# Performance work log

Measured on AMD Instinct MI355X. Metric: run time of the kernel, lower is better.

The kernel has to match this reference:

```python
import jax, jax.numpy as jnp
import numpy as np

N = 50000      # nodes
E = 800000     # edges
CIN = 128
CH = 128
COUT = 64
EPS = 1e-5     # BatchNorm eps


def setup_inputs() -> dict:
    key = jax.random.key(0)
    ks = jax.random.split(key, 16)
    s = 0.1  # weight scale for numerical stability
    return {
        "x": jax.random.normal(ks[0], (N, CIN), jnp.float32),
        "edge_index": jax.random.randint(ks[1], (2, E), 0, N, jnp.int32),
        "edge_weights": jax.random.uniform(ks[2], (E,), jnp.float32),
        "w1": jax.random.normal(ks[3], (CIN, CH), jnp.float32) * s,
        "b1": jnp.zeros((CH,), jnp.float32),
        "bn1_g": jnp.ones((CH,), jnp.float32),
        "bn1_b": jnp.zeros((CH,), jnp.float32),
        "bn1_m": jax.random.normal(ks[4], (CH,), jnp.float32) * 0.1,
        "bn1_v": jax.random.uniform(ks[5], (CH,), jnp.float32) + 0.5,
        "conv_ws": jax.random.normal(ks[6], (2, CH, CH), jnp.float32) * s,
        "conv_bs": jnp.zeros((2, CH), jnp.float32),
        "bns_g": jnp.ones((2, CH), jnp.float32),
        "bns_b": jnp.zeros((2, CH), jnp.float32),
        "bns_m": jax.random.normal(ks[7], (2, CH), jnp.float32) * 0.1,
        "bns_v": jax.random.uniform(ks[8], (2, CH), jnp.float32) + 0.5,
        "lin1_w": jax.random.normal(ks[9], (CH, CH), jnp.float32) * s,
        "lin1_b": jnp.zeros((CH,), jnp.float32),
        "lin2_w": jax.random.normal(ks[10], (CH, COUT), jnp.float32) * s,
        "lin2_b": jnp.zeros((COUT,), jnp.float32),
    }


def _bn(h, g, b, m, v):
    # BatchNorm1d in eval mode: running statistics
    return (h - m) * jax.lax.rsqrt(v + EPS) * g + b


def _gcn(h, w, b, src, dst, norm, n):
    # GCNConv: out[dst] += norm_e * (h @ W)[src]  (self loops already in src/dst)
    h = h @ w
    msg = h[src] * norm[:, None]                 # [E+N, CH]
    return jax.ops.segment_sum(msg, dst, num_segments=n) + b


def reference(x, edge_index, edge_weights, w1, b1, bn1_g, bn1_b, bn1_m, bn1_v,
              conv_ws, conv_bs, bns_g, bns_b, bns_m, bns_v,
              lin1_w, lin1_b, lin2_w, lin2_b):
    n = x.shape[0]
    loop = jnp.arange(n, dtype=edge_index.dtype)
    src = jnp.concatenate([edge_index[0], loop])
    dst = jnp.concatenate([edge_index[1], loop])
    ew = jnp.concatenate([edge_weights, jnp.ones((n,), edge_weights.dtype)])
    # symmetric degree normalization (PyG gcn_norm)
    deg = jax.ops.segment_sum(ew, dst, num_segments=n)
    dis = jnp.where(deg > 0, jax.lax.rsqrt(deg), 0.0)
    norm = dis[src] * ew * dis[dst]

    lrelu = jax.nn.leaky_relu  # slope 0.01, matches F.leaky_relu default
    h = lrelu(_bn(_gcn(x, w1, b1, src, dst, norm, n), bn1_g, bn1_b, bn1_m, bn1_v))
    for i in range(conv_ws.shape[0]):
        h = lrelu(_bn(_gcn(h, conv_ws[i], conv_bs[i], src, dst, norm, n),
                      bns_g[i], bns_b[i], bns_m[i], bns_v[i]) + h)
    h = lrelu(h @ lin1_w + lin1_b)
    # dropout is identity in eval mode
    return h @ lin2_w + lin2_b
```

## Files before the change

### kernel.cpp

```cpp
#include <hip/hip_runtime.h>
#include <hip/hip_bf16.h>


constexpr int   NN    = 50000;
constexpr int   EE    = 800000;
constexpr int   CH    = 128;
constexpr int   SLOTS = 64;
constexpr int   NBUK  = 782;
constexpr int   RCAP  = 2048;
constexpr int   EPB   = 2048;
constexpr int   NB_BIN = (EE + EPB - 1) / EPB;
constexpr int   NB_WZ  = (73728 + 384 + 255) / 256;
constexpr float EPS   = 1e-5f;

typedef __attribute__((ext_vector_type(8))) short bf16x8;
typedef __attribute__((ext_vector_type(4))) float f32x4;
typedef unsigned long long u64;
typedef unsigned short u16;

__device__ inline u16 f2bf_rne(float f) {
  unsigned u = __float_as_uint(f);
  unsigned r = u + 0x7fffu + ((u >> 16) & 1u);
  return (u16)(r >> 16);
}
__device__ inline float bf2f(unsigned h16) {
  return __uint_as_float(h16 << 16);
}


__global__ __launch_bounds__(256) void binw_kernel(
    const int* __restrict__ ei, const float* __restrict__ ew,
    unsigned* __restrict__ gcur, u64* __restrict__ bins,
    const float* __restrict__ w1, const float* __restrict__ bn1_g, const float* __restrict__ bn1_v,
    const float* __restrict__ conv_ws, const float* __restrict__ bns_g, const float* __restrict__ bns_v,
    const float* __restrict__ lin1_w, const float* __restrict__ lin2_w,
    const float* __restrict__ b1, const float* __restrict__ bn1_b, const float* __restrict__ bn1_m,
    const float* __restrict__ conv_bs, const float* __restrict__ bns_b, const float* __restrict__ bns_m,
    u16* __restrict__ w1h, u16* __restrict__ w1l,
    u16* __restrict__ c0h, u16* __restrict__ c0l,
    u16* __restrict__ c1h, u16* __restrict__ c1l,
    u16* __restrict__ l1h, u16* __restrict__ l1l,
    u16* __restrict__ l2h, u16* __restrict__ l2l,
    float* __restrict__ beff)
{
  const int tid = threadIdx.x;
  if (blockIdx.x >= NB_BIN) {
    int idx = (blockIdx.x - NB_BIN) * 256 + tid;
    if (idx >= 73728) {
      int r = idx - 73728;
      if (r >= 384) return;
      int l = r >> 7, c = r & 127;
      float bc, gg, bb, mm, vv;
      if (l == 0) { bc = b1[c]; gg = bn1_g[c]; bb = bn1_b[c]; mm = bn1_m[c]; vv = bn1_v[c]; }
      else {
        int o = (l - 1) * 128 + c;
        bc = conv_bs[o]; gg = bns_g[o]; bb = bns_b[o]; mm = bns_m[o]; vv = bns_v[o];
      }
      beff[r] = (bc - mm) * gg * rsqrtf(vv + EPS) + bb;
      return;
    }
    const float* W; const float* g = nullptr; const float* v = nullptr;
    u16 *hi, *lo; int CO = 128; int local;
    if      (idx < 16384) { W = w1;              g = bn1_g;     v = bn1_v;     hi = w1h; lo = w1l; local = idx; }
    else if (idx < 32768) { W = conv_ws;         g = bns_g;     v = bns_v;     hi = c0h; lo = c0l; local = idx - 16384; }
    else if (idx < 49152) { W = conv_ws + 16384; g = bns_g+128; v = bns_v+128; hi = c1h; lo = c1l; local = idx - 32768; }
    else if (idx < 65536) { W = lin1_w;                                        hi = l1h; lo = l1l; local = idx - 49152; }
    else                  { W = lin2_w;                                        hi = l2h; lo = l2l; local = idx - 65536; CO = 64; }
    int k = local / CO, n = local % CO;
    float w = W[local];
    if (g) w *= g[n] * rsqrtf(v[n] + EPS);
    int NCT = CO / 16;
    int kchunk = k >> 5, kin = k & 31, quad = kin >> 3, j = kin & 7;
    int ct = n >> 4, l = (quad << 4) | (n & 15);
    size_t pos = ((size_t)(kchunk * NCT + ct) * 64 + l) * 8 + j;
    u16 h = f2bf_rne(w);
    hi[pos] = h;
    lo[pos] = f2bf_rne(w - bf2f(h));
    return;
  }
  __shared__ unsigned cnt[NBUK];
  __shared__ unsigned base[NBUK];
  for (int b = tid; b < NBUK; b += 256) cnt[b] = 0;
  __syncthreads();
  const int e0 = blockIdx.x * EPB;
  unsigned pk[8]; u16 bkt[8]; u16 rnk[8]; unsigned char dl[8];
  #pragma unroll
  for (int i = 0; i < 8; i++) {
    int e = e0 + i * 256 + tid;
    if (e < EE) {
      int s = ei[e], d = ei[EE + e];
      float w = ew[e];
      bkt[i] = (u16)(d >> 6);
      dl[i]  = (unsigned char)(d & 63);
      pk[i]  = ((unsigned)f2bf_rne(w) << 16) | (unsigned)s;
      rnk[i] = (u16)atomicAdd(&cnt[bkt[i]], 1u);
    } else bkt[i] = 0xffffu;
  }
  __syncthreads();
  for (int b = tid; b < NBUK; b += 256) {
    unsigned c = cnt[b];
    base[b] = c ? atomicAdd(&gcur[b * 16], c) : 0u;
  }
  __syncthreads();
  #pragma unroll
  for (int i = 0; i < 8; i++) {
    if (bkt[i] == 0xffffu) continue;
    unsigned pos = base[bkt[i]] + rnk[i];
    if (pos < RCAP)
      bins[(size_t)bkt[i] * RCAP + pos] = ((u64)dl[i] << 32) | pk[i];
  }
}


__global__ __launch_bounds__(256) void scatgemm_kernel(
    const unsigned* __restrict__ gcur, const u64* __restrict__ bins,
    unsigned* __restrict__ ell, float* __restrict__ dis,
    const float* __restrict__ Ain,
    const u16* __restrict__ Whi, const u16* __restrict__ Wlo,
    u16* __restrict__ Cout)
{
  __shared__ unsigned rank[64];
  __shared__ float    wsum[64];
  __shared__ float    disl[64];
  __shared__ float    lds[64][CH + 4];
  const int b   = blockIdx.x;
  const int tid = threadIdx.x;

  if (tid < 64) { rank[tid] = 1u; wsum[tid] = 0.f; }
  __syncthreads();
  unsigned cnt = gcur[b * 16];
  if (cnt > RCAP) cnt = RCAP;
  const u64* src = bins + (size_t)b * RCAP;
  for (unsigned i = tid; i < cnt; i += 256) {
    u64 v = src[i];
    unsigned pk = (unsigned)v;
    unsigned dl = (unsigned)(v >> 32);
    unsigned r = atomicAdd(&rank[dl], 1u);
    if (r < SLOTS)
      ell[((size_t)(b * 64 + dl)) * SLOTS + r] = pk;
    atomicAdd(&wsum[dl], bf2f(pk >> 16));
  }
  __syncthreads();
  if (tid < 64) {
    int node = b * 64 + tid;
    float d = rsqrtf(1.0f + wsum[tid]);
    disl[tid] = d;
    if (node < NN) {
      unsigned c = rank[tid];
      if (c > SLOTS) c = SLOTS;
      ell[(size_t)node * SLOTS] = c;
      dis[node] = d;
    }
  }
  __syncthreads();

  const int wave = tid >> 6;
  const int lane = tid & 63;
  const int quad = lane >> 4;
  const int mrow = lane & 15;
  const int row0 = b * 64;

  int arow = row0 + wave * 16 + mrow;
  if (arow >= NN) arow = NN - 1;

  bf16x8 ahi[4], alo[4];
  const float* Ar = Ain + (size_t)arow * CH;
  #pragma unroll
  for (int c = 0; c < 4; c++) {
    int off = c * 32 + quad * 8;
    float4 f0 = *(const float4*)(Ar + off);
    float4 f1 = *(const float4*)(Ar + off + 4);
    float f[8] = {f0.x, f0.y, f0.z, f0.w, f1.x, f1.y, f1.z, f1.w};
    #pragma unroll
    for (int j = 0; j < 8; j++) {
      u16 h = f2bf_rne(f[j]);
      ahi[c][j] = (short)h;
      alo[c][j] = (short)f2bf_rne(f[j] - bf2f(h));
    }
  }

  f32x4 acc[8];
  #pragma unroll
  for (int t = 0; t < 8; t++) acc[t] = (f32x4){0.f, 0.f, 0.f, 0.f};
  #pragma unroll
  for (int c = 0; c < 4; c++) {
    #pragma unroll
    for (int t = 0; t < 8; t++) {
      size_t base = ((size_t)(c * 8 + t) * 64 + lane) * 8;
      bf16x8 bh = *(const bf16x8*)(Whi + base);
      bf16x8 bl = *(const bf16x8*)(Wlo + base);
      acc[t] = __builtin_amdgcn_mfma_f32_16x16x32_bf16(ahi[c], bh, acc[t], 0, 0, 0);
      acc[t] = __builtin_amdgcn_mfma_f32_16x16x32_bf16(alo[c], bh, acc[t], 0, 0, 0);
      acc[t] = __builtin_amdgcn_mfma_f32_16x16x32_bf16(ahi[c], bl, acc[t], 0, 0, 0);
    }
  }

  #pragma unroll
  for (int t = 0; t < 8; t++)
    #pragma unroll
    for (int r = 0; r < 4; r++)
      lds[wave * 16 + quad * 4 + r][t * 16 + mrow] = acc[t][r];
  __syncthreads();

  #pragma unroll
  for (int i = tid; i < 64 * CH / 4; i += 256) {
    int row = (i * 4) / CH;
    int col = (i * 4) % CH;
    int grow = row0 + row;
    if (grow >= NN) continue;
    float rs = disl[row];
    const float* lp = &lds[row][col];
    u16* cp = (u16*)Cout + (size_t)grow * CH + col;
    unsigned p0 = ((unsigned)f2bf_rne(lp[1] * rs) << 16) | f2bf_rne(lp[0] * rs);
    unsigned p1 = ((unsigned)f2bf_rne(lp[3] * rs) << 16) | f2bf_rne(lp[2] * rs);
    *(uint2*)cp = make_uint2(p0, p1);
  }
}

template<bool RES, bool WH>
__device__ __forceinline__ void gather4_qw(
    const u16* __restrict__ hwin, const unsigned* __restrict__ ell,
    const float* __restrict__ dis, const float* __restrict__ beff,
    const u16* __restrict__ res, u16* __restrict__ hout,
    unsigned* __restrict__ hsbase,
    int nbase, int lane, int sub, int grp)
{
  int nd0 = nbase < NN ? nbase : NN - 1;
  unsigned wcur = ell[(size_t)nd0 * SLOTS + lane];
  for (int r = 0; r < 4; r++) {
    int node = nbase + r;
    int nd = node < NN ? node : NN - 1;
    unsigned myword = wcur;
    if (r < 3) {
      int n2 = node + 1 < NN ? node + 1 : NN - 1;
      wcur = ell[(size_t)n2 * SLOTS + lane];
    }
    int cnt = __shfl((int)myword, 0);
    if (cnt > SLOTS) cnt = SLOTS;
    float a[8] = {0.f, 0.f, 0.f, 0.f, 0.f, 0.f, 0.f, 0.f};
    for (int j = 0; j < cnt; j += 32) {
      unsigned sidx[8]; float wv[8];
      #pragma unroll
      for (int q = 0; q < 8; q++) {
        int jj = j + q * 4 + grp;
        unsigned e = (unsigned)__shfl((int)myword, jj & 63);
        float    w = (jj == 0) ? 1.0f : bf2f(e >> 16);
        unsigned s = (jj == 0) ? (unsigned)nd : (e & 0xffffu);
        if (jj >= cnt) { w = 0.f; s = (unsigned)nd; }
        sidx[q] = s; wv[q] = w;
      }
      uint4 h[8];
      #pragma unroll
      for (int q = 0; q < 8; q++)
        h[q] = *(const uint4*)(hwin + (size_t)sidx[q] * CH + sub * 8);
      __builtin_amdgcn_sched_group_barrier(0x20 , 8, 0);
      #pragma unroll
      for (int q = 0; q < 8; q++) {
        float w = wv[q];
        a[0] = fmaf(w, bf2f(h[q].x & 0xffffu), a[0]); a[1] = fmaf(w, bf2f(h[q].x >> 16), a[1]);
        a[2] = fmaf(w, bf2f(h[q].y & 0xffffu), a[2]); a[3] = fmaf(w, bf2f(h[q].y >> 16), a[3]);
        a[4] = fmaf(w, bf2f(h[q].z & 0xffffu), a[4]); a[5] = fmaf(w, bf2f(h[q].z >> 16), a[5]);
        a[6] = fmaf(w, bf2f(h[q].w & 0xffffu), a[6]); a[7] = fmaf(w, bf2f(h[q].w >> 16), a[7]);
      }
    }
    #pragma unroll
    for (int k = 0; k < 8; k++) {
      a[k] += __shfl_xor(a[k], 16);
      a[k] += __shfl_xor(a[k], 32);
    }
    if (grp == 0) {
      float disd = dis[nd];
      int c = sub * 8;
      float4 be0 = *(const float4*)(beff + c);
      float4 be1 = *(const float4*)(beff + c + 4);
      float y[8];
      y[0] = a[0] * disd + be0.x; y[1] = a[1] * disd + be0.y;
      y[2] = a[2] * disd + be0.z; y[3] = a[3] * disd + be0.w;
      y[4] = a[4] * disd + be1.x; y[5] = a[5] * disd + be1.y;
      y[6] = a[6] * disd + be1.z; y[7] = a[7] * disd + be1.w;
      if constexpr (RES) {
        uint4 rr = *(const uint4*)(res + (size_t)nd * CH + c);
        y[0] += bf2f(rr.x & 0xffffu); y[1] += bf2f(rr.x >> 16);
        y[2] += bf2f(rr.y & 0xffffu); y[3] += bf2f(rr.y >> 16);
        y[4] += bf2f(rr.z & 0xffffu); y[5] += bf2f(rr.z >> 16);
        y[6] += bf2f(rr.w & 0xffffu); y[7] += bf2f(rr.w >> 16);
      }
      #pragma unroll
      for (int k = 0; k < 8; k++) y[k] = y[k] > 0.f ? y[k] : 0.01f * y[k];
      uint4 o;
      o.x = ((unsigned)f2bf_rne(y[1]) << 16) | f2bf_rne(y[0]);
      o.y = ((unsigned)f2bf_rne(y[3]) << 16) | f2bf_rne(y[2]);
      o.z = ((unsigned)f2bf_rne(y[5]) << 16) | f2bf_rne(y[4]);
      o.w = ((unsigned)f2bf_rne(y[7]) << 16) | f2bf_rne(y[6]);
      if constexpr (WH) {
        if (node < NN) *(uint4*)(hout + (size_t)node * CH + c) = o;
      }
      *(uint4*)&hsbase[r * 68 + sub * 4] = o;
    }
  }
}

template<bool RES>
__global__ __launch_bounds__(256, 4) void fuse_kernel(
    const u16* __restrict__ hwin,
    const unsigned* __restrict__ ell, const float* __restrict__ dis,
    const float* __restrict__ beff, const u16* __restrict__ res,
    const u16* __restrict__ Whi, const u16* __restrict__ Wlo,
    u16* __restrict__ hout, u16* __restrict__ hwout)
{
  __shared__ unsigned hs[16][68];
  const int tid  = threadIdx.x;
  const int wave = tid >> 6;
  const int lane = tid & 63;
  const int sub  = lane & 15;
  const int grp  = lane >> 4;
  const int row0 = blockIdx.x * 16;

  gather4_qw<RES, true>(hwin, ell, dis, beff, res, hout,
                        &hs[wave * 4][0], row0 + wave * 4, lane, sub, grp);
  __syncthreads();

  bf16x8 af[4];
  #pragma unroll
  for (int c = 0; c < 4; c++)
    af[c] = *(const bf16x8*)&hs[sub][c * 16 + grp * 4];
  __syncthreads();

  f32x4 acc[2];
  #pragma unroll
  for (int t = 0; t < 2; t++) acc[t] = (f32x4){0.f, 0.f, 0.f, 0.f};
  #pragma unroll
  for (int c = 0; c < 4; c++) {
    #pragma unroll
    for (int t = 0; t < 2; t++) {
      size_t base = ((size_t)(c * 8 + wave * 2 + t) * 64 + lane) * 8;
      bf16x8 bh = *(const bf16x8*)(Whi + base);
      bf16x8 bl = *(const bf16x8*)(Wlo + base);
      acc[t] = __builtin_amdgcn_mfma_f32_16x16x32_bf16(af[c], bh, acc[t], 0, 0, 0);
      acc[t] = __builtin_amdgcn_mfma_f32_16x16x32_bf16(af[c], bl, acc[t], 0, 0, 0);
    }
  }

  u16* hs16 = (u16*)&hs[0][0];
  #pragma unroll
  for (int r = 0; r < 4; r++) {
    int row = grp * 4 + r;
    float rs = dis[row0 + row];
    #pragma unroll
    for (int t = 0; t < 2; t++)
      hs16[row * 136 + wave * 32 + t * 16 + sub] = f2bf_rne(acc[t][r] * rs);
  }
  __syncthreads();
  {
    int row   = tid >> 4;
    int chunk = tid & 15;
    uint4 o = *(const uint4*)(hs16 + row * 136 + chunk * 8);
    *(uint4*)(hwout + (size_t)(row0 + row) * CH + chunk * 8) = o;
  }
}

__global__ __launch_bounds__(256, 4) void fuse_last_kernel(
    const u16* __restrict__ hwin,
    const unsigned* __restrict__ ell, const float* __restrict__ dis,
    const float* __restrict__ beff, const u16* __restrict__ res,
    const u16* __restrict__ l1h, const u16* __restrict__ l1l,
    const float* __restrict__ b1,
    const u16* __restrict__ l2h, const u16* __restrict__ l2l,
    const float* __restrict__ b2, float* __restrict__ out)
{
  __shared__ unsigned hs[16][68];
  __shared__ float    fs[16][132];
  const int tid  = threadIdx.x;
  const int wave = tid >> 6;
  const int lane = tid & 63;
  const int sub  = lane & 15;
  const int grp  = lane >> 4;
  const int row0 = blockIdx.x * 16;

  gather4_qw<true, false>(hwin, ell, dis, beff, res, nullptr,
                          &hs[wave * 4][0], row0 + wave * 4, lane, sub, grp);
  __syncthreads();

  bf16x8 af[4];
  #pragma unroll
  for (int c = 0; c < 4; c++)
    af[c] = *(const bf16x8*)&hs[sub][c * 16 + grp * 4];

  f32x4 acc[2];
  #pragma unroll
  for (int t = 0; t < 2; t++) acc[t] = (f32x4){0.f, 0.f, 0.f, 0.f};
  #pragma unroll
  for (int c = 0; c < 4; c++) {
    #pragma unroll
    for (int t = 0; t < 2; t++) {
      size_t base = ((size_t)(c * 8 + wave * 2 + t) * 64 + lane) * 8;
      bf16x8 bh = *(const bf16x8*)(l1h + base);
      bf16x8 bl = *(const bf16x8*)(l1l + base);
      acc[t] = __builtin_amdgcn_mfma_f32_16x16x32_bf16(af[c], bh, acc[t], 0, 0, 0);
      acc[t] = __builtin_amdgcn_mfma_f32_16x16x32_bf16(af[c], bl, acc[t], 0, 0, 0);
    }
  }
  #pragma unroll
  for (int t = 0; t < 2; t++) {
    int col = wave * 32 + t * 16 + sub;
    float bb = b1[col];
    #pragma unroll
    for (int r = 0; r < 4; r++) {
      float x = acc[t][r] + bb;
      x = x > 0.f ? x : 0.01f * x;
      fs[grp * 4 + r][col] = x;
    }
  }
  __syncthreads();

  f32x4 acc2 = (f32x4){0.f, 0.f, 0.f, 0.f};
  #pragma unroll
  for (int c = 0; c < 4; c++) {
    bf16x8 ahi, alo;
    const float* lp = &fs[sub][c * 32 + grp * 8];
    float4 f0 = *(const float4*)lp;
    float4 f1 = *(const float4*)(lp + 4);
    float f[8] = {f0.x, f0.y, f0.z, f0.w, f1.x, f1.y, f1.z, f1.w};
    #pragma unroll
    for (int j = 0; j < 8; j++) {
      u16 h = f2bf_rne(f[j]);
      ahi[j] = (short)h;
      alo[j] = (short)f2bf_rne(f[j] - bf2f(h));
    }
    size_t base = ((size_t)(c * 4 + wave) * 64 + lane) * 8;
    bf16x8 bh = *(const bf16x8*)(l2h + base);
    bf16x8 bl = *(const bf16x8*)(l2l + base);
    acc2 = __builtin_amdgcn_mfma_f32_16x16x32_bf16(ahi, bh, acc2, 0, 0, 0);
    acc2 = __builtin_amdgcn_mfma_f32_16x16x32_bf16(alo, bh, acc2, 0, 0, 0);
    acc2 = __builtin_amdgcn_mfma_f32_16x16x32_bf16(ahi, bl, acc2, 0, 0, 0);
  }
  {
    float bb = b2[wave * 16 + sub];
    #pragma unroll
    for (int r = 0; r < 4; r++) {
      int grow = row0 + grp * 4 + r;
      if (grow < NN)
        out[(size_t)grow * 64 + wave * 16 + sub] = acc2[r] + bb;
    }
  }
}


extern "C" void kernel_launch(void* const* d_in, const int* in_sizes, int n_in,
                              void* d_out, int out_size, void* d_ws, size_t ws_size,
                              hipStream_t stream) {
  const float* x       = (const float*)d_in[0];
  const int*   ei      = (const int*)  d_in[1];
  const float* ew      = (const float*)d_in[2];
  const float* w1      = (const float*)d_in[3];
  const float* b1      = (const float*)d_in[4];
  const float* bn1_g   = (const float*)d_in[5];
  const float* bn1_b   = (const float*)d_in[6];
  const float* bn1_m   = (const float*)d_in[7];
  const float* bn1_v   = (const float*)d_in[8];
  const float* conv_ws = (const float*)d_in[9];
  const float* conv_bs = (const float*)d_in[10];
  const float* bns_g   = (const float*)d_in[11];
  const float* bns_b   = (const float*)d_in[12];
  const float* bns_m   = (const float*)d_in[13];
  const float* bns_v   = (const float*)d_in[14];
  const float* lin1_w  = (const float*)d_in[15];
  const float* lin1_b  = (const float*)d_in[16];
  const float* lin2_w  = (const float*)d_in[17];
  const float* lin2_b  = (const float*)d_in[18];
  float* out = (float*)d_out;

  size_t off = 0;
  auto alloc = [&](size_t elems) -> void* {
    void* p = (char*)d_ws + off * 4;
    off += (elems + 3) & ~(size_t)3;
    return p;
  };
  unsigned* gcur = (unsigned*)alloc(NBUK * 16);
  u64*      bins = (u64*)     alloc((size_t)NBUK * RCAP * 2);
  unsigned* ell  = (unsigned*)alloc((size_t)NN * SLOTS);
  float*    dis  = (float*)   alloc(NN);
  float*    beff = (float*)   alloc(3 * CH);
  u16*      hwa  = (u16*)     alloc((size_t)NN * CH / 2);
  u16*      hwb  = (u16*)     alloc((size_t)NN * CH / 2);
  u16*      h1   = (u16*)     alloc((size_t)NN * CH / 2);
  u16*      h2   = (u16*)     alloc((size_t)NN * CH / 2);
  u16* w1h = (u16*)alloc(CH * CH / 2); u16* w1l = (u16*)alloc(CH * CH / 2);
  u16* c0h = (u16*)alloc(CH * CH / 2); u16* c0l = (u16*)alloc(CH * CH / 2);
  u16* c1h = (u16*)alloc(CH * CH / 2); u16* c1l = (u16*)alloc(CH * CH / 2);
  u16* l1h = (u16*)alloc(CH * CH / 2); u16* l1l = (u16*)alloc(CH * CH / 2);
  u16* l2h = (u16*)alloc(CH * 64 / 2); u16* l2l = (u16*)alloc(CH * 64 / 2);

  const int nb_fuse = (NN + 15) / 16;
  dim3 B(256);

  hipMemsetAsync(gcur, 0, NBUK * 16 * sizeof(unsigned), stream);

  binw_kernel<<<NB_BIN + NB_WZ, B, 0, stream>>>(ei, ew, gcur, bins,
      w1, bn1_g, bn1_v, conv_ws, bns_g, bns_v, lin1_w, lin2_w,
      b1, bn1_b, bn1_m, conv_bs, bns_b, bns_m,
      w1h, w1l, c0h, c0l, c1h, c1l, l1h, l1l, l2h, l2l, beff);

  scatgemm_kernel<<<NBUK, B, 0, stream>>>(gcur, bins, ell, dis, x, w1h, w1l, hwa);

  fuse_kernel<false><<<nb_fuse, B, 0, stream>>>(hwa, ell, dis, beff, nullptr,
      c0h, c0l, h1, hwb);

  fuse_kernel<true><<<nb_fuse, B, 0, stream>>>(hwb, ell, dis, beff + CH, h1,
      c1h, c1l, h2, hwa);

  fuse_last_kernel<<<nb_fuse, B, 0, stream>>>(hwa, ell, dis, beff + 2 * CH, h2,
      l1h, l1l, lin1_b, l2h, l2l, lin2_b, out);
}
```

Baseline: 303.2 us.

## Split gathered feature matrix into two 64-column halves for cache-friendlier gathers

Stores the transformed node features (h@W scaled) as two separate N×64 planes instead of one N×128 array, and gathers each half in a separate pass with 8-byte loads per lane. The intent is to shrink the working set touched by the random neighbour gather in each pass so it fits better in L2/MALL and to reduce register pressure, which also lets launch bounds rise to 6 blocks per SM. The trade-off is that the edge list is walked twice, a block-wide barrier is added inside the gather helper, and the bounds clamp on the last nodes is removed.

Result: slower. 358.7 us (+18.3%).

```diff
diff --git a/kernel.cpp b/kernel.cpp
--- a/kernel.cpp
+++ b/kernel.cpp
@@ -12,6 +12,7 @@
 constexpr int   NB_BIN = (EE + EPB - 1) / EPB;
 constexpr int   NB_WZ  = (73728 + 384 + 255) / 256;
 constexpr float EPS   = 1e-5f;
+constexpr size_t HHALF = (size_t)NN * 64;
 
 typedef __attribute__((ext_vector_type(8))) short bf16x8;
 typedef __attribute__((ext_vector_type(4))) float f32x4;
@@ -210,7 +211,8 @@
     if (grow >= NN) continue;
     float rs = disl[row];
     const float* lp = &lds[row][col];
-    u16* cp = (u16*)Cout + (size_t)grow * CH + col;
+    int half = col >> 6, lcol = col & 63;
+    u16* cp = Cout + (size_t)half * HHALF + (size_t)grow * 64 + lcol;
     unsigned p0 = ((unsigned)f2bf_rne(lp[1] * rs) << 16) | f2bf_rne(lp[0] * rs);
     unsigned p1 = ((unsigned)f2bf_rne(lp[3] * rs) << 16) | f2bf_rne(lp[2] * rs);
     *(uint2*)cp = make_uint2(p0, p1);
@@ -218,90 +220,85 @@
 }
 
 template<bool RES, bool WH>
-__device__ __forceinline__ void gather4_qw(
+__device__ __forceinline__ void gather4_split(
     const u16* __restrict__ hwin, const unsigned* __restrict__ ell,
     const float* __restrict__ dis, const float* __restrict__ beff,
     const u16* __restrict__ res, u16* __restrict__ hout,
     unsigned* __restrict__ hsbase,
     int nbase, int lane, int sub, int grp)
 {
-  int nd0 = nbase < NN ? nbase : NN - 1;
-  unsigned wcur = ell[(size_t)nd0 * SLOTS + lane];
-  for (int r = 0; r < 4; r++) {
-    int node = nbase + r;
-    int nd = node < NN ? node : NN - 1;
-    unsigned myword = wcur;
-    if (r < 3) {
-      int n2 = node + 1 < NN ? node + 1 : NN - 1;
-      wcur = ell[(size_t)n2 * SLOTS + lane];
-    }
-    int cnt = __shfl((int)myword, 0);
-    if (cnt > SLOTS) cnt = SLOTS;
-    float a[8] = {0.f, 0.f, 0.f, 0.f, 0.f, 0.f, 0.f, 0.f};
-    for (int j = 0; j < cnt; j += 32) {
-      unsigned sidx[8]; float wv[8];
-      #pragma unroll
-      for (int q = 0; q < 8; q++) {
-        int jj = j + q * 4 + grp;
-        unsigned e = (unsigned)__shfl((int)myword, jj & 63);
-        float    w = (jj == 0) ? 1.0f : bf2f(e >> 16);
-        unsigned s = (jj == 0) ? (unsigned)nd : (e & 0xffffu);
-        if (jj >= cnt) { w = 0.f; s = (unsigned)nd; }
-        sidx[q] = s; wv[q] = w;
-      }
-      uint4 h[8];
-      #pragma unroll
-      for (int q = 0; q < 8; q++)
-        h[q] = *(const uint4*)(hwin + (size_t)sidx[q] * CH + sub * 8);
-      __builtin_amdgcn_sched_group_barrier(0x20 , 8, 0);
-      #pragma unroll
-      for (int q = 0; q < 8; q++) {
-        float w = wv[q];
-        a[0] = fmaf(w, bf2f(h[q].x & 0xffffu), a[0]); a[1] = fmaf(w, bf2f(h[q].x >> 16), a[1]);
-        a[2] = fmaf(w, bf2f(h[q].y & 0xffffu), a[2]); a[3] = fmaf(w, bf2f(h[q].y >> 16), a[3]);
-        a[4] = fmaf(w, bf2f(h[q].z & 0xffffu), a[4]); a[5] = fmaf(w, bf2f(h[q].z >> 16), a[5]);
-        a[6] = fmaf(w, bf2f(h[q].w & 0xffffu), a[6]); a[7] = fmaf(w, bf2f(h[q].w >> 16), a[7]);
-      }
-    }
-    #pragma unroll
-    for (int k = 0; k < 8; k++) {
-      a[k] += __shfl_xor(a[k], 16);
-      a[k] += __shfl_xor(a[k], 32);
-    }
-    if (grp == 0) {
-      float disd = dis[nd];
-      int c = sub * 8;
-      float4 be0 = *(const float4*)(beff + c);
-      float4 be1 = *(const float4*)(beff + c + 4);
-      float y[8];
-      y[0] = a[0] * disd + be0.x; y[1] = a[1] * disd + be0.y;
-      y[2] = a[2] * disd + be0.z; y[3] = a[3] * disd + be0.w;
-      y[4] = a[4] * disd + be1.x; y[5] = a[5] * disd + be1.y;
-      y[6] = a[6] * disd + be1.z; y[7] = a[7] * disd + be1.w;
-      if constexpr (RES) {
-        uint4 rr = *(const uint4*)(res + (size_t)nd * CH + c);
-        y[0] += bf2f(rr.x & 0xffffu); y[1] += bf2f(rr.x >> 16);
-        y[2] += bf2f(rr.y & 0xffffu); y[3] += bf2f(rr.y >> 16);
-        y[4] += bf2f(rr.z & 0xffffu); y[5] += bf2f(rr.z >> 16);
-        y[6] += bf2f(rr.w & 0xffffu); y[7] += bf2f(rr.w >> 16);
+  unsigned wr[4];
+  #pragma unroll
+  for (int r = 0; r < 4; r++)
+    wr[r] = ell[(size_t)(nbase + r) * SLOTS + lane];
+
+  #pragma unroll
+  for (int h = 0; h < 2; h++) {
+    const u16* hbase = hwin + (size_t)h * HHALF + sub * 4;
+    #pragma unroll
+    for (int r = 0; r < 4; r++) {
+      const int nd = nbase + r;
+      unsigned myword = wr[r];
+      int cnt = __shfl((int)myword, 0);
+      if (cnt > SLOTS) cnt = SLOTS;
+      float a[4] = {0.f, 0.f, 0.f, 0.f};
+      for (int j = 0; j < cnt; j += 32) {
+        unsigned sidx[8]; float wv[8];
+        #pragma unroll
+        for (int q = 0; q < 8; q++) {
+          int jj = j + q * 4 + grp;
+          unsigned e = (unsigned)__shfl((int)myword, jj & 63);
+          float    w = (jj == 0) ? 1.0f : bf2f(e >> 16);
+          unsigned s = (jj == 0) ? (unsigned)nd : (e & 0xffffu);
+          if (jj >= cnt) { w = 0.f; s = (unsigned)nd; }
+          sidx[q] = s; wv[q] = w;
+        }
+        uint2 hv[8];
+        #pragma unroll
+        for (int q = 0; q < 8; q++)
+          hv[q] = *(const uint2*)(hbase + (size_t)sidx[q] * 64);
+        #pragma unroll
+        for (int q = 0; q < 8; q++) {
+          float w = wv[q];
+          a[0] = fmaf(w, bf2f(hv[q].x & 0xffffu), a[0]);
+          a[1] = fmaf(w, bf2f(hv[q].x >> 16),     a[1]);
+          a[2] = fmaf(w, bf2f(hv[q].y & 0xffffu), a[2]);
+          a[3] = fmaf(w, bf2f(hv[q].y >> 16),     a[3]);
+        }
       }
       #pragma unroll
-      for (int k = 0; k < 8; k++) y[k] = y[k] > 0.f ? y[k] : 0.01f * y[k];
-      uint4 o;
-      o.x = ((unsigned)f2bf_rne(y[1]) << 16) | f2bf_rne(y[0]);
-      o.y = ((unsigned)f2bf_rne(y[3]) << 16) | f2bf_rne(y[2]);
-      o.z = ((unsigned)f2bf_rne(y[5]) << 16) | f2bf_rne(y[4]);
-      o.w = ((unsigned)f2bf_rne(y[7]) << 16) | f2bf_rne(y[6]);
-      if constexpr (WH) {
-        if (node < NN) *(uint4*)(hout + (size_t)node * CH + c) = o;
+      for (int k = 0; k < 4; k++) {
+        a[k] += __shfl_xor(a[k], 16);
+        a[k] += __shfl_xor(a[k], 32);
       }
-      *(uint4*)&hsbase[r * 68 + sub * 4] = o;
-    }
+      if (grp == 0) {
+        float disd = dis[nd];
+        int c = h * 64 + sub * 4;
+        float4 be = *(const float4*)(beff + c);
+        float y[4];
+        y[0] = a[0] * disd + be.x; y[1] = a[1] * disd + be.y;
+        y[2] = a[2] * disd + be.z; y[3] = a[3] * disd + be.w;
+        if constexpr (RES) {
+          uint2 rr = *(const uint2*)(res + (size_t)nd * CH + c);
+          y[0] += bf2f(rr.x & 0xffffu); y[1] += bf2f(rr.x >> 16);
+          y[2] += bf2f(rr.y & 0xffffu); y[3] += bf2f(rr.y >> 16);
+        }
+        #pragma unroll
+        for (int k = 0; k < 4; k++) y[k] = y[k] > 0.f ? y[k] : 0.01f * y[k];
+        uint2 o;
+        o.x = ((unsigned)f2bf_rne(y[1]) << 16) | f2bf_rne(y[0]);
+        o.y = ((unsigned)f2bf_rne(y[3]) << 16) | f2bf_rne(y[2]);
+        if constexpr (WH)
+          *(uint2*)(hout + (size_t)nd * CH + c) = o;
+        *(uint2*)&hsbase[r * 68 + h * 32 + sub * 2] = o;
+      }
+    }
+    __syncthreads();
   }
 }
 
 template<bool RES>
-__global__ __launch_bounds__(256, 4) void fuse_kernel(
+__global__ __launch_bounds__(256, 6) void fuse_kernel(
     const u16* __restrict__ hwin,
     const unsigned* __restrict__ ell, const float* __restrict__ dis,
     const float* __restrict__ beff, const u16* __restrict__ res,
@@ -316,8 +313,8 @@
   const int grp  = lane >> 4;
   const int row0 = blockIdx.x * 16;
 
-  gather4_qw<RES, true>(hwin, ell, dis, beff, res, hout,
-                        &hs[wave * 4][0], row0 + wave * 4, lane, sub, grp);
+  gather4_split<RES, true>(hwin, ell, dis, beff, res, hout,
+                           &hs[wave * 4][0], row0 + wave * 4, lane, sub, grp);
   __syncthreads();
 
   bf16x8 af[4];
@@ -355,11 +352,12 @@
     int row   = tid >> 4;
     int chunk = tid & 15;
     uint4 o = *(const uint4*)(hs16 + row * 136 + chunk * 8);
-    *(uint4*)(hwout + (size_t)(row0 + row) * CH + chunk * 8) = o;
-  }
-}
-
-__global__ __launch_bounds__(256, 4) void fuse_last_kernel(
+    int half = chunk >> 3;
+    *(uint4*)(hwout + (size_t)half * HHALF + (size_t)(row0 + row) * 64 + (chunk & 7) * 8) = o;
+  }
+}
+
+__global__ __launch_bounds__(256, 6) void fuse_last_kernel(
     const u16* __restrict__ hwin,
     const unsigned* __restrict__ ell, const float* __restrict__ dis,
     const float* __restrict__ beff, const u16* __restrict__ res,
@@ -377,8 +375,8 @@
   const int grp  = lane >> 4;
   const int row0 = blockIdx.x * 16;
 
-  gather4_qw<true, false>(hwin, ell, dis, beff, res, nullptr,
-                          &hs[wave * 4][0], row0 + wave * 4, lane, sub, grp);
+  gather4_split<true, false>(hwin, ell, dis, beff, res, nullptr,
+                             &hs[wave * 4][0], row0 + wave * 4, lane, sub, grp);
   __syncthreads();
 
   bf16x8 af[4];
```
